# Optimization experiments

Measured on AMD Instinct MI355X. Metric: run time of the kernel, lower is better.

## Reference

```python
import jax, jax.numpy as jnp
import numpy as np

XY = 16   # xy_size
Z = 16    # z_size
S = XY * XY * Z   # num_states = 4096
V = 2048  # num_tokens


def _build_structure():
    # Static 3D-grid neighbor structure (replaces the per-state Python loop).
    h = np.arange(S)
    zc, rem = np.divmod(h, XY * XY)
    yc, xc = np.divmod(rem, XY)
    coords = np.stack([xc, yc, zc], 1)                       # [S,3] (x,y,z)
    offs = np.array([[0, 0, 0], [1, 0, 0], [-1, 0, 0], [0, 1, 0],
                     [0, -1, 0], [0, 0, 1], [0, 0, 2]])       # 7 fixed offsets
    nc = coords[:, None, :] + offs[None]                      # [S,7,3]
    valid = ((nc[..., 0] >= 0) & (nc[..., 0] < XY) &
             (nc[..., 1] >= 0) & (nc[..., 1] < XY) &
             (nc[..., 2] >= 0) & (nc[..., 2] < Z))
    dest = nc[..., 0] + XY * (nc[..., 1] + XY * nc[..., 2])   # flat neighbor idx
    # compact valid neighbors to the front, preserving offset order:
    # j-th valid neighbor consumes logit j (matches logits[h, :len(valid)])
    order = np.argsort(~valid, axis=1, kind='stable')
    tgt = np.take_along_axis(dest, order, axis=1)
    vmask = np.take_along_axis(valid, order, axis=1)
    tgt = np.where(vmask, tgt, S)  # invalid slots -> dummy column S
    return jnp.asarray(tgt), jnp.asarray(vmask)

TGT, VMASK = _build_structure()


def transition_log_p(trans_w):
    # masked log-softmax over the first k valid logits of each row
    logits = jnp.where(VMASK, trans_w, -1e30)
    logp = jax.nn.log_softmax(logits, axis=1)
    logp = jnp.where(VMASK, logp, -jnp.inf)
    T = jnp.full((S, S + 1), -jnp.inf, trans_w.dtype)
    T = T.at[jnp.arange(S)[:, None], TGT].set(logp)
    return T[:, :S]  # [S,S], row h = log p(transition targets of h)


def smoothed_emission(emis_w):
    em = jax.nn.log_softmax(emis_w, axis=-1).reshape(Z, XY, XY, V)
    lv, rv = em[:, :, :1], em[:, :, -1:]
    lh, rh = em[:, :1], em[:, -1:]
    c = jnp.zeros((Z, 1, 1, V), em.dtype)  # log(1)=0 pad, as in the original
    c2 = lambda *a: jnp.concatenate(a, axis=2)
    c1 = lambda *a: jnp.concatenate(a, axis=1)
    up = c1(c2(lv, em, rv), c2(c, rh, c), c2(c, rh, c))
    dn = c1(c2(c, lh, c), c2(c, lh, c), c2(lv, em, rv))
    lf = c1(c2(lh, c, c), c2(em, rv, rv), c2(rh, c, c))
    rt = c1(c2(c, c, lh), c2(lv, lv, em), c2(c, c, rh))
    cr = c1(c2(c, lh, c), c2(lv, em, rv), c2(c, rh, c))
    mean = jax.nn.logsumexp(jnp.stack((up, dn, lf, rt, cr)), axis=0) - jnp.log(5.0)
    return mean[:, 1:-1, 1:-1].reshape(S, V)


def _forward(stories, trans_w, emis_w, prior_w):
    priors = jax.nn.log_softmax(prior_w)                      # [S]
    em = smoothed_emission(emis_w)                            # [S,V]
    padded = jnp.concatenate([em, jnp.zeros((S, 1), em.dtype)], axis=1)  # [S,V+1]
    # per-(story, step) emission log-prob: sum over sentence tokens
    all_emis = padded.T[stories].sum(axis=2)                  # [B,L,S]
    all_emis = jnp.transpose(all_emis, (1, 0, 2))             # [L,B,S]
    T = transition_log_p(trans_w)                             # [S,S]
    amax = jnp.max(T, axis=1, keepdims=True)                  # [S,1], finite (self-loop)
    P = jnp.exp(T - amax)                                     # [S,S]
    score0 = all_emis[0] + priors                             # [B,S]

    def step(score, em_t):
        # new[b,a] = em_t[b,a] + logsumexp_h(T[a,h] + score[b,h])  (stable log-matmul)
        smax = jnp.max(score, axis=1, keepdims=True)          # [B,1]
        new = em_t + jnp.log(jnp.exp(score - smax) @ P.T) + smax + amax.T
        return new, new

    _, rest = jax.lax.scan(step, score0, all_emis[1:])
    return jnp.concatenate([score0[None], rest], axis=0)      # [L,B,S]


def setup_inputs() -> dict:
    key = jax.random.key(0)
    k1, k2, k3, k4 = jax.random.split(key, 4)
    B, L, W = 8, 32, 8
    return {
        "stories_tensor": jax.random.randint(k1, (B, L, W), 0, V + 1, dtype=jnp.int32),
        "story_length": L,
        "trans_w": jax.random.normal(k2, (S, 7), jnp.float32),
        "emis_w": jax.random.normal(k3, (S, V), jnp.float32),
        "prior_w": jax.random.normal(k4, (S,), jnp.float32),
    }


def reference(stories_tensor, story_length, trans_w, emis_w, prior_w):
    assert stories_tensor.shape[1] == story_length
    return _forward(stories_tensor, trans_w, emis_w, prior_w)
```

## Files before the change

### kernel.cpp

```cpp
#include <hip/hip_runtime.h>
#include <math.h>

#define XYD 16
#define ZD 16
#define SS 4096
#define VV 2048
#define BB 8
#define LL 32
#define WW 8
#define VC 32
#define SM_STRIDE 257

#define GUARD_L 16
#define GUARD_R 512
#define EBUF_N (GUARD_L + SS + GUARD_R)

#define BAR() asm volatile("s_waitcnt lgkmcnt(0)\n\ts_barrier" ::: "memory")

__device__ __forceinline__ float b2f(unsigned short u) {
    union { unsigned int i; float f; } x; x.i = ((unsigned int)u) << 16; return x.f;
}
__device__ __forceinline__ unsigned short f2b(float f) {
    union { float f; unsigned int i; } x; x.f = f; return (unsigned short)(x.i >> 16);
}

__global__ void k_logZ(const float* __restrict__ emis_w, float* __restrict__ logZ) {
    int wave = threadIdx.x >> 6;
    int lane = threadIdx.x & 63;
    int row  = blockIdx.x * 4 + wave;
    const float* r = emis_w + (size_t)row * VV;
    float vals[32];
    float m = -INFINITY;
#pragma unroll
    for (int k = 0; k < 8; k++) {
        float4 f = ((const float4*)r)[k * 64 + lane];
        vals[k*4+0] = f.x; vals[k*4+1] = f.y; vals[k*4+2] = f.z; vals[k*4+3] = f.w;
    }
#pragma unroll
    for (int k = 0; k < 32; k++) m = fmaxf(m, vals[k]);
#pragma unroll
    for (int o = 32; o; o >>= 1) m = fmaxf(m, __shfl_xor(m, o));
    float sum = 0.f;
#pragma unroll
    for (int k = 0; k < 32; k++) sum += __expf(vals[k] - m);
#pragma unroll
    for (int o = 32; o; o >>= 1) sum += __shfl_xor(sum, o);
    if (lane == 0) logZ[row] = m + __logf(sum);
}

__global__ void k_smooth(const float* __restrict__ emis_w, const float* __restrict__ logZ,
                         unsigned short* __restrict__ smTb) {
    __shared__ float tileT[VC * SM_STRIDE];
    int z  = blockIdx.x;
    int v0 = blockIdx.y * VC;
    int tid = threadIdx.x;
    int rsub = tid >> 3;
    int c0   = (tid & 7) * 4;

#pragma unroll
    for (int it = 0; it < 8; it++) {
        int r  = it * 32 + rsub;
        int sg = z * 256 + r;
        float lz = logZ[sg];
        float4 w = *(const float4*)(emis_w + (size_t)sg * VV + v0 + c0);
        tileT[(c0+0)*SM_STRIDE + r] = __expf(w.x - lz);
        tileT[(c0+1)*SM_STRIDE + r] = __expf(w.y - lz);
        tileT[(c0+2)*SM_STRIDE + r] = __expf(w.z - lz);
        tileT[(c0+3)*SM_STRIDE + r] = __expf(w.w - lz);
    }
    __syncthreads();

    int x = tid & 15, y = tid >> 4;
    int sxp = (x < 15) ? tid + 1  : tid;
    int sxm = (x > 0)  ? tid - 1  : tid;
    int syp = (y < 15) ? tid + 16 : tid;
    int sym = (y > 0)  ? tid - 16 : tid;
    unsigned short* o = smTb + (size_t)v0 * SS + z * 256 + tid;
#pragma unroll
    for (int i = 0; i < VC; i++) {
        const float* tb = tileT + i * SM_STRIDE;
        float s = tb[tid] + tb[sxp] + tb[sxm] + tb[syp] + tb[sym];
        o[(size_t)i * SS] = f2b(__logf(s * 0.2f));
    }
}

__global__ void __launch_bounds__(1024) k_forward(
    const float* __restrict__ trans_w, const float* __restrict__ prior_w,
    const unsigned short* __restrict__ smTb, const int* __restrict__ stories,
    float* __restrict__ out) {
    __shared__ __align__(16) unsigned short Ebuf[2][EBUF_N];
    __shared__ float red2[2];
    __shared__ float pr[16];
    __shared__ int toksL[LL * WW];
    int b = blockIdx.x;
    int tid = threadIdx.x;
    int lane = tid & 63, wid = tid >> 6;

    if (tid < GUARD_L) { Ebuf[0][tid] = 0; Ebuf[1][tid] = 0; }
    if (tid < GUARD_R) {
        Ebuf[0][GUARD_L + SS + tid] = 0;
        Ebuf[1][GUARD_L + SS + tid] = 0;
    }
    if (tid < LL * WW) toksL[tid] = stories[b * LL * WW + tid];

    float pw[28], am[4];
    {
        float w7[28];
        const float4* t4 = (const float4*)(trans_w + (size_t)tid * 28);
#pragma unroll
        for (int k = 0; k < 7; k++) ((float4*)w7)[k] = t4[k];
#pragma unroll
        for (int i = 0; i < 4; i++) {
            int j = tid * 4 + i;
            int xx = j & 15, yy = (j >> 4) & 15, zz = j >> 8;
            bool val[7];
            val[0] = true;
            val[1] = (xx < 15); val[2] = (xx > 0);
            val[3] = (yy < 15); val[4] = (yy > 0);
            val[5] = (zz < 15); val[6] = (zz < 14);
            const float* rw = w7 + i * 7;
            float w[7]; int cnt = 0; float m = -INFINITY;
#pragma unroll
            for (int d = 0; d < 7; d++) { if (val[d]) { w[d] = rw[cnt++]; m = fmaxf(m, w[d]); } }
            float se = 0.f;
#pragma unroll
            for (int d = 0; d < 7; d++) if (val[d]) se += __expf(w[d] - m);
#pragma unroll
            for (int d = 0; d < 7; d++) pw[i*7+d] = val[d] ? __expf(w[d] - m) : 0.f;
            am[i] = -__logf(se);
        }
    }

    float4 pv = ((const float4*)prior_w)[tid];
    __syncthreads();

    const unsigned short* smBase = smTb + 4 * tid;
    float4 em = {0.f, 0.f, 0.f, 0.f};
#pragma unroll
    for (int w = 0; w < WW; w++) {
        int tk = toksL[w];
        if (tk < VV) {
            ushort4 u = *(const ushort4*)(smBase + (size_t)tk * SS);
            em.x += b2f(u.x); em.y += b2f(u.y); em.z += b2f(u.z); em.w += b2f(u.w);
        }
    }

    float lm = fmaxf(fmaxf(pv.x, pv.y), fmaxf(pv.z, pv.w));
#pragma unroll
    for (int o = 32; o; o >>= 1) lm = fmaxf(lm, __shfl_xor(lm, o));
    if (lane == 0) pr[wid] = lm;
    __syncthreads();
    float gm = pr[0];
#pragma unroll
    for (int w = 1; w < 16; w++) gm = fmaxf(gm, pr[w]);
    __syncthreads();
    float ls = __expf(pv.x - gm) + __expf(pv.y - gm) + __expf(pv.z - gm) + __expf(pv.w - gm);
#pragma unroll
    for (int o = 32; o; o >>= 1) ls += __shfl_xor(ls, o);
    if (lane == 0) pr[wid] = ls;
    __syncthreads();
    float gs = 0.f;
#pragma unroll
    for (int w = 0; w < 16; w++) gs += pr[w];
    float logZp = gm + __logf(gs);

    float v0 = em.x + pv.x - logZp;
    float v1 = em.y + pv.y - logZp;
    float v2 = em.z + pv.z - logZp;
    float v3 = em.w + pv.w - logZp;
    float4 ov_prev = {v0, v1, v2, v3};
    float4* outp = (float4*)(out + (size_t)b * SS) + tid;

    if (tid == 0) red2[0] = v0;
    __syncthreads();
    float g1 = red2[0];
    float XpPrev = g1;
    float E0 = __expf(v0 - XpPrev), E1 = __expf(v1 - XpPrev);
    float E2 = __expf(v2 - XpPrev), E3 = __expf(v3 - XpPrev);
    {
        ushort4 E;
        E.x = f2b(E0); E.y = f2b(E1); E.z = f2b(E2); E.w = f2b(E3);
        *(ushort4*)(&Ebuf[0][GUARD_L + 4 * tid]) = E;
    }

    ushort4 pf[WW];
#pragma unroll
    for (int w = 0; w < WW; w++) {
        int tk = toksL[WW + w];
        pf[w] = (tk < VV) ? *(const ushort4*)(smBase + (size_t)tk * SS)
                          : (ushort4){0, 0, 0, 0};
    }

    int cur = 0;
    for (int t = 1; t < LL; t++) {
        BAR();
        em.x = 0.f; em.y = 0.f; em.z = 0.f; em.w = 0.f;
#pragma unroll
        for (int w = 0; w < WW; w++) {
            em.x += b2f(pf[w].x); em.y += b2f(pf[w].y);
            em.z += b2f(pf[w].z); em.w += b2f(pf[w].w);
        }
        if (t < LL - 1) {
#pragma unroll
            for (int w = 0; w < WW; w++) {
                int tk = toksL[(t + 1) * WW + w];
                pf[w] = (tk < VV) ? *(const ushort4*)(smBase + (size_t)tk * SS)
                                  : (ushort4){0, 0, 0, 0};
            }
        }

        float g0 = red2[cur];
        float Xp = 2.f * g0 - g1;
        float dX = XpPrev - Xp;
        float F0 = __expf(em.x + am[0] + dX);
        float F1 = __expf(em.y + am[1] + dX);
        float F2 = __expf(em.z + am[2] + dX);
        float F3 = __expf(em.w + am[3] + dX);

        *outp = ov_prev;
        outp += (BB * SS) / 4;

        const unsigned short* Eb = Ebuf[cur] + GUARD_L + 4 * tid;
        ushort4 YpU = *(const ushort4*)(Eb + 16);
        ushort4 YmU = *(const ushort4*)(Eb - 16);
        ushort4 ZpU = *(const ushort4*)(Eb + 256);
        ushort4 ZqU = *(const ushort4*)(Eb + 512);
        float bx  = b2f(Eb[4]);
        float cxw = b2f(Eb[-1]);

        float a0 = E0*pw[0]  + E1*pw[1]  + cxw*pw[2] + b2f(YpU.x)*pw[3]  + b2f(YmU.x)*pw[4]  + b2f(ZpU.x)*pw[5]  + b2f(ZqU.x)*pw[6];
        float a1 = E1*pw[7]  + E2*pw[8]  + E0*pw[9]  + b2f(YpU.y)*pw[10] + b2f(YmU.y)*pw[11] + b2f(ZpU.y)*pw[12] + b2f(ZqU.y)*pw[13];
        float a2 = E2*pw[14] + E3*pw[15] + E1*pw[16] + b2f(YpU.z)*pw[17] + b2f(YmU.z)*pw[18] + b2f(ZpU.z)*pw[19] + b2f(ZqU.z)*pw[20];
        float a3 = E3*pw[21] + bx*pw[22] + E2*pw[23] + b2f(YpU.w)*pw[24] + b2f(YmU.w)*pw[25] + b2f(ZpU.w)*pw[26] + b2f(ZqU.w)*pw[27];

        E0 = a0 * F0; E1 = a1 * F1; E2 = a2 * F2; E3 = a3 * F3;
        {
            ushort4 E;
            E.x = f2b(E0); E.y = f2b(E1); E.z = f2b(E2); E.w = f2b(E3);
            *(ushort4*)(&Ebuf[cur ^ 1][GUARD_L + 4 * tid]) = E;
        }
        float lg0 = __logf(a0);
        if (tid == 0) red2[cur ^ 1] = em.x + lg0 + XpPrev + am[0];

        ov_prev.x = em.x + lg0        + XpPrev + am[0];
        ov_prev.y = em.y + __logf(a1) + XpPrev + am[1];
        ov_prev.z = em.z + __logf(a2) + XpPrev + am[2];
        ov_prev.w = em.w + __logf(a3) + XpPrev + am[3];

        g1 = g0; XpPrev = Xp; cur ^= 1;
    }
    *outp = ov_prev;
}

extern "C" void kernel_launch(void* const* d_in, const int* in_sizes, int n_in,
                              void* d_out, int out_size, void* d_ws, size_t ws_size,
                              hipStream_t stream) {
    const int*   stories = (const int*)d_in[0];
    const float* trans_w = (const float*)d_in[2];
    const float* emis_w  = (const float*)d_in[3];
    const float* prior_w = (const float*)d_in[4];
    float* out = (float*)d_out;

    char* ws = (char*)d_ws;
    unsigned short* smTb = (unsigned short*)(ws);
    float* logZ = (float*)(ws + (size_t)VV * SS * 2);

    k_logZ<<<SS / 4, 256, 0, stream>>>(emis_w, logZ);
    k_smooth<<<dim3(ZD, VV / VC), 256, 0, stream>>>(emis_w, logZ, smTb);
    k_forward<<<BB, 1024, 0, stream>>>(trans_w, prior_w, smTb, stories, out);
}
```

Before: 183.7 us.

## Fuse all stages into one cooperative kernel with grid syncs and precomputed emissions

Replaces three kernel launches with a single cooperative kernel of 256 blocks that runs logZ, the smoothing transpose and an emission gather across the whole grid, separated by grid.sync. The per-timestep emission sums are computed in parallel by all blocks into a workspace buffer, so the sequential forward loop on 8 blocks only reads one float4 per step instead of gathering eight bf16 rows. This removes launch gaps and takes the gather off the serial critical path. In exchange it adds grid-wide barriers, a requirement that all 256 blocks of 1024 threads be co-resident, and an extra global write and read of all emissions.

After: 247.1 us. 34.5% more time.

```diff
diff --git a/kernel.cpp b/kernel.cpp
--- a/kernel.cpp
+++ b/kernel.cpp
@@ -1,5 +1,8 @@
 #include <hip/hip_runtime.h>
+#include <hip/hip_cooperative_groups.h>
 #include <math.h>
+
+namespace cg = cooperative_groups;
 
 #define XYD 16
 #define ZD 16
@@ -24,232 +27,237 @@
     union { float f; unsigned int i; } x; x.f = f; return (unsigned short)(x.i >> 16);
 }
 
-__global__ void k_logZ(const float* __restrict__ emis_w, float* __restrict__ logZ) {
-    int wave = threadIdx.x >> 6;
-    int lane = threadIdx.x & 63;
-    int row  = blockIdx.x * 4 + wave;
-    const float* r = emis_w + (size_t)row * VV;
-    float vals[32];
-    float m = -INFINITY;
-#pragma unroll
-    for (int k = 0; k < 8; k++) {
-        float4 f = ((const float4*)r)[k * 64 + lane];
-        vals[k*4+0] = f.x; vals[k*4+1] = f.y; vals[k*4+2] = f.z; vals[k*4+3] = f.w;
-    }
-#pragma unroll
-    for (int k = 0; k < 32; k++) m = fmaxf(m, vals[k]);
-#pragma unroll
-    for (int o = 32; o; o >>= 1) m = fmaxf(m, __shfl_xor(m, o));
-    float sum = 0.f;
-#pragma unroll
-    for (int k = 0; k < 32; k++) sum += __expf(vals[k] - m);
-#pragma unroll
-    for (int o = 32; o; o >>= 1) sum += __shfl_xor(sum, o);
-    if (lane == 0) logZ[row] = m + __logf(sum);
-}
-
-__global__ void k_smooth(const float* __restrict__ emis_w, const float* __restrict__ logZ,
-                         unsigned short* __restrict__ smTb) {
-    __shared__ float tileT[VC * SM_STRIDE];
-    int z  = blockIdx.x;
-    int v0 = blockIdx.y * VC;
-    int tid = threadIdx.x;
-    int rsub = tid >> 3;
-    int c0   = (tid & 7) * 4;
-
-#pragma unroll
-    for (int it = 0; it < 8; it++) {
-        int r  = it * 32 + rsub;
-        int sg = z * 256 + r;
-        float lz = logZ[sg];
-        float4 w = *(const float4*)(emis_w + (size_t)sg * VV + v0 + c0);
-        tileT[(c0+0)*SM_STRIDE + r] = __expf(w.x - lz);
-        tileT[(c0+1)*SM_STRIDE + r] = __expf(w.y - lz);
-        tileT[(c0+2)*SM_STRIDE + r] = __expf(w.z - lz);
-        tileT[(c0+3)*SM_STRIDE + r] = __expf(w.w - lz);
-    }
-    __syncthreads();
-
-    int x = tid & 15, y = tid >> 4;
-    int sxp = (x < 15) ? tid + 1  : tid;
-    int sxm = (x > 0)  ? tid - 1  : tid;
-    int syp = (y < 15) ? tid + 16 : tid;
-    int sym = (y > 0)  ? tid - 16 : tid;
-    unsigned short* o = smTb + (size_t)v0 * SS + z * 256 + tid;
-#pragma unroll
-    for (int i = 0; i < VC; i++) {
-        const float* tb = tileT + i * SM_STRIDE;
-        float s = tb[tid] + tb[sxp] + tb[sxm] + tb[syp] + tb[sym];
-        o[(size_t)i * SS] = f2b(__logf(s * 0.2f));
-    }
-}
-
-__global__ void __launch_bounds__(1024) k_forward(
-    const float* __restrict__ trans_w, const float* __restrict__ prior_w,
-    const unsigned short* __restrict__ smTb, const int* __restrict__ stories,
-    float* __restrict__ out) {
-    __shared__ __align__(16) unsigned short Ebuf[2][EBUF_N];
-    __shared__ float red2[2];
-    __shared__ float pr[16];
-    __shared__ int toksL[LL * WW];
-    int b = blockIdx.x;
-    int tid = threadIdx.x;
+__global__ void __launch_bounds__(1024, 4) k_all(
+    const int* __restrict__ stories, const float* __restrict__ trans_w,
+    const float* __restrict__ emis_w, const float* __restrict__ prior_w,
+    float* __restrict__ out, unsigned short* __restrict__ smTb,
+    float* __restrict__ all_emis, float* __restrict__ logZ) {
+
+    __shared__ __align__(16) char shraw[VC * SM_STRIDE * sizeof(float)];
+
+    cg::grid_group grid = cg::this_grid();
+    int tid = threadIdx.x, bid = blockIdx.x;
     int lane = tid & 63, wid = tid >> 6;
 
-    if (tid < GUARD_L) { Ebuf[0][tid] = 0; Ebuf[1][tid] = 0; }
-    if (tid < GUARD_R) {
-        Ebuf[0][GUARD_L + SS + tid] = 0;
-        Ebuf[1][GUARD_L + SS + tid] = 0;
-    }
-    if (tid < LL * WW) toksL[tid] = stories[b * LL * WW + tid];
-
-    float pw[28], am[4];
-    {
-        float w7[28];
-        const float4* t4 = (const float4*)(trans_w + (size_t)tid * 28);
-#pragma unroll
-        for (int k = 0; k < 7; k++) ((float4*)w7)[k] = t4[k];
-#pragma unroll
-        for (int i = 0; i < 4; i++) {
-            int j = tid * 4 + i;
-            int xx = j & 15, yy = (j >> 4) & 15, zz = j >> 8;
-            bool val[7];
-            val[0] = true;
-            val[1] = (xx < 15); val[2] = (xx > 0);
-            val[3] = (yy < 15); val[4] = (yy > 0);
-            val[5] = (zz < 15); val[6] = (zz < 14);
-            const float* rw = w7 + i * 7;
-            float w[7]; int cnt = 0; float m = -INFINITY;
-#pragma unroll
-            for (int d = 0; d < 7; d++) { if (val[d]) { w[d] = rw[cnt++]; m = fmaxf(m, w[d]); } }
-            float se = 0.f;
-#pragma unroll
-            for (int d = 0; d < 7; d++) if (val[d]) se += __expf(w[d] - m);
-#pragma unroll
-            for (int d = 0; d < 7; d++) pw[i*7+d] = val[d] ? __expf(w[d] - m) : 0.f;
-            am[i] = -__logf(se);
-        }
-    }
-
-    float4 pv = ((const float4*)prior_w)[tid];
-    __syncthreads();
-
-    const unsigned short* smBase = smTb + 4 * tid;
-    float4 em = {0.f, 0.f, 0.f, 0.f};
-#pragma unroll
-    for (int w = 0; w < WW; w++) {
-        int tk = toksL[w];
-        if (tk < VV) {
-            ushort4 u = *(const ushort4*)(smBase + (size_t)tk * SS);
-            em.x += b2f(u.x); em.y += b2f(u.y); em.z += b2f(u.z); em.w += b2f(u.w);
-        }
-    }
-
-    float lm = fmaxf(fmaxf(pv.x, pv.y), fmaxf(pv.z, pv.w));
-#pragma unroll
-    for (int o = 32; o; o >>= 1) lm = fmaxf(lm, __shfl_xor(lm, o));
-    if (lane == 0) pr[wid] = lm;
-    __syncthreads();
-    float gm = pr[0];
-#pragma unroll
-    for (int w = 1; w < 16; w++) gm = fmaxf(gm, pr[w]);
-    __syncthreads();
-    float ls = __expf(pv.x - gm) + __expf(pv.y - gm) + __expf(pv.z - gm) + __expf(pv.w - gm);
-#pragma unroll
-    for (int o = 32; o; o >>= 1) ls += __shfl_xor(ls, o);
-    if (lane == 0) pr[wid] = ls;
-    __syncthreads();
-    float gs = 0.f;
-#pragma unroll
-    for (int w = 0; w < 16; w++) gs += pr[w];
-    float logZp = gm + __logf(gs);
-
-    float v0 = em.x + pv.x - logZp;
-    float v1 = em.y + pv.y - logZp;
-    float v2 = em.z + pv.z - logZp;
-    float v3 = em.w + pv.w - logZp;
-    float4 ov_prev = {v0, v1, v2, v3};
-    float4* outp = (float4*)(out + (size_t)b * SS) + tid;
-
-    if (tid == 0) red2[0] = v0;
-    __syncthreads();
-    float g1 = red2[0];
-    float XpPrev = g1;
-    float E0 = __expf(v0 - XpPrev), E1 = __expf(v1 - XpPrev);
-    float E2 = __expf(v2 - XpPrev), E3 = __expf(v3 - XpPrev);
-    {
-        ushort4 E;
-        E.x = f2b(E0); E.y = f2b(E1); E.z = f2b(E2); E.w = f2b(E3);
-        *(ushort4*)(&Ebuf[0][GUARD_L + 4 * tid]) = E;
-    }
-
-    ushort4 pf[WW];
-#pragma unroll
-    for (int w = 0; w < WW; w++) {
-        int tk = toksL[WW + w];
-        pf[w] = (tk < VV) ? *(const ushort4*)(smBase + (size_t)tk * SS)
-                          : (ushort4){0, 0, 0, 0};
-    }
-
-    int cur = 0;
-    for (int t = 1; t < LL; t++) {
-        BAR();
-        em.x = 0.f; em.y = 0.f; em.z = 0.f; em.w = 0.f;
+    {
+        int row = bid * 16 + wid;
+        const float* r = emis_w + (size_t)row * VV;
+        float vals[32];
+        float m = -INFINITY;
+#pragma unroll
+        for (int k = 0; k < 8; k++) {
+            float4 f = ((const float4*)r)[k * 64 + lane];
+            vals[k*4+0] = f.x; vals[k*4+1] = f.y; vals[k*4+2] = f.z; vals[k*4+3] = f.w;
+        }
+#pragma unroll
+        for (int k = 0; k < 32; k++) m = fmaxf(m, vals[k]);
+#pragma unroll
+        for (int o = 32; o; o >>= 1) m = fmaxf(m, __shfl_xor(m, o));
+        float sum = 0.f;
+#pragma unroll
+        for (int k = 0; k < 32; k++) sum += __expf(vals[k] - m);
+#pragma unroll
+        for (int o = 32; o; o >>= 1) sum += __shfl_xor(sum, o);
+        if (lane == 0) logZ[row] = m + __logf(sum);
+    }
+    grid.sync();
+
+    {
+        float* tileT = (float*)shraw;
+        int rsub = tid >> 3;
+        int c0   = (tid & 7) * 4;
+        int s    = tid & 255, g = tid >> 8;
+        int x = s & 15, y = s >> 4;
+        int sxp = (x < 15) ? s + 1  : s;
+        int sxm = (x > 0)  ? s - 1  : s;
+        int syp = (y < 15) ? s + 16 : s;
+        int sym = (y > 0)  ? s - 16 : s;
+#pragma unroll
+        for (int c = 0; c < 4; c++) {
+            int combo = bid * 4 + c;
+            int z  = combo >> 6;
+            int v0 = (combo & 63) * VC;
+            __syncthreads();
+#pragma unroll
+            for (int it = 0; it < 2; it++) {
+                int r  = it * 128 + rsub;
+                int sg = z * 256 + r;
+                float lz = logZ[sg];
+                float4 w = *(const float4*)(emis_w + (size_t)sg * VV + v0 + c0);
+                tileT[(c0+0)*SM_STRIDE + r] = __expf(w.x - lz);
+                tileT[(c0+1)*SM_STRIDE + r] = __expf(w.y - lz);
+                tileT[(c0+2)*SM_STRIDE + r] = __expf(w.z - lz);
+                tileT[(c0+3)*SM_STRIDE + r] = __expf(w.w - lz);
+            }
+            __syncthreads();
+            unsigned short* o = smTb + (size_t)(v0 + g * 8) * SS + z * 256 + s;
+#pragma unroll
+            for (int i = 0; i < 8; i++) {
+                const float* tb = tileT + (g * 8 + i) * SM_STRIDE;
+                float sm = tb[s] + tb[sxp] + tb[sxm] + tb[syp] + tb[sym];
+                o[(size_t)i * SS] = f2b(__logf(sm * 0.2f));
+            }
+        }
+    }
+    grid.sync();
+
+    {
+        int t = bid >> 3, b = bid & 7;
+        int tok[WW];
+#pragma unroll
+        for (int w = 0; w < WW; w++) tok[w] = stories[(b * LL + t) * WW + w];
+        int s0 = tid * 4;
+        float4 acc = {0.f, 0.f, 0.f, 0.f};
 #pragma unroll
         for (int w = 0; w < WW; w++) {
-            em.x += b2f(pf[w].x); em.y += b2f(pf[w].y);
-            em.z += b2f(pf[w].z); em.w += b2f(pf[w].w);
-        }
-        if (t < LL - 1) {
-#pragma unroll
-            for (int w = 0; w < WW; w++) {
-                int tk = toksL[(t + 1) * WW + w];
-                pf[w] = (tk < VV) ? *(const ushort4*)(smBase + (size_t)tk * SS)
-                                  : (ushort4){0, 0, 0, 0};
-            }
-        }
-
-        float g0 = red2[cur];
-        float Xp = 2.f * g0 - g1;
-        float dX = XpPrev - Xp;
-        float F0 = __expf(em.x + am[0] + dX);
-        float F1 = __expf(em.y + am[1] + dX);
-        float F2 = __expf(em.z + am[2] + dX);
-        float F3 = __expf(em.w + am[3] + dX);
-
-        *outp = ov_prev;
-        outp += (BB * SS) / 4;
-
-        const unsigned short* Eb = Ebuf[cur] + GUARD_L + 4 * tid;
-        ushort4 YpU = *(const ushort4*)(Eb + 16);
-        ushort4 YmU = *(const ushort4*)(Eb - 16);
-        ushort4 ZpU = *(const ushort4*)(Eb + 256);
-        ushort4 ZqU = *(const ushort4*)(Eb + 512);
-        float bx  = b2f(Eb[4]);
-        float cxw = b2f(Eb[-1]);
-
-        float a0 = E0*pw[0]  + E1*pw[1]  + cxw*pw[2] + b2f(YpU.x)*pw[3]  + b2f(YmU.x)*pw[4]  + b2f(ZpU.x)*pw[5]  + b2f(ZqU.x)*pw[6];
-        float a1 = E1*pw[7]  + E2*pw[8]  + E0*pw[9]  + b2f(YpU.y)*pw[10] + b2f(YmU.y)*pw[11] + b2f(ZpU.y)*pw[12] + b2f(ZqU.y)*pw[13];
-        float a2 = E2*pw[14] + E3*pw[15] + E1*pw[16] + b2f(YpU.z)*pw[17] + b2f(YmU.z)*pw[18] + b2f(ZpU.z)*pw[19] + b2f(ZqU.z)*pw[20];
-        float a3 = E3*pw[21] + bx*pw[22] + E2*pw[23] + b2f(YpU.w)*pw[24] + b2f(YmU.w)*pw[25] + b2f(ZpU.w)*pw[26] + b2f(ZqU.w)*pw[27];
-
-        E0 = a0 * F0; E1 = a1 * F1; E2 = a2 * F2; E3 = a3 * F3;
+            if (tok[w] < VV) {
+                ushort4 u = *(const ushort4*)(smTb + (size_t)tok[w] * SS + s0);
+                acc.x += b2f(u.x); acc.y += b2f(u.y);
+                acc.z += b2f(u.z); acc.w += b2f(u.w);
+            }
+        }
+        *(float4*)(all_emis + ((size_t)t * BB + b) * SS + s0) = acc;
+    }
+    grid.sync();
+
+    if (bid >= BB) return;
+    {
+        unsigned short* Eb0 = (unsigned short*)shraw;
+        unsigned short* Eb1 = Eb0 + EBUF_N;
+        float* red2 = (float*)(shraw + 4 * EBUF_N);
+        float* pr   = red2 + 2;
+        int b = bid;
+
+        if (tid < GUARD_L) { Eb0[tid] = 0; Eb1[tid] = 0; }
+        if (tid < GUARD_R) {
+            Eb0[GUARD_L + SS + tid] = 0;
+            Eb1[GUARD_L + SS + tid] = 0;
+        }
+
+        float pw[28], am[4];
+        {
+            float w7[28];
+            const float4* t4 = (const float4*)(trans_w + (size_t)tid * 28);
+#pragma unroll
+            for (int k = 0; k < 7; k++) ((float4*)w7)[k] = t4[k];
+#pragma unroll
+            for (int i = 0; i < 4; i++) {
+                int j = tid * 4 + i;
+                int xx = j & 15, yy = (j >> 4) & 15, zz = j >> 8;
+                bool val[7];
+                val[0] = true;
+                val[1] = (xx < 15); val[2] = (xx > 0);
+                val[3] = (yy < 15); val[4] = (yy > 0);
+                val[5] = (zz < 15); val[6] = (zz < 14);
+                const float* rw = w7 + i * 7;
+                float w[7]; int cnt = 0; float m = -INFINITY;
+#pragma unroll
+                for (int d = 0; d < 7; d++) { if (val[d]) { w[d] = rw[cnt++]; m = fmaxf(m, w[d]); } }
+                float se = 0.f;
+#pragma unroll
+                for (int d = 0; d < 7; d++) if (val[d]) se += __expf(w[d] - m);
+#pragma unroll
+                for (int d = 0; d < 7; d++) pw[i*7+d] = val[d] ? __expf(w[d] - m) : 0.f;
+                am[i] = -__logf(se);
+            }
+        }
+
+        float4 pv = ((const float4*)prior_w)[tid];
+        const float4* emp = (const float4*)(all_emis + (size_t)b * SS) + tid;
+        float4 em = *emp;
+
+        float lm = fmaxf(fmaxf(pv.x, pv.y), fmaxf(pv.z, pv.w));
+#pragma unroll
+        for (int o = 32; o; o >>= 1) lm = fmaxf(lm, __shfl_xor(lm, o));
+        if (lane == 0) pr[wid] = lm;
+        __syncthreads();
+        float gm = pr[0];
+#pragma unroll
+        for (int w = 1; w < 16; w++) gm = fmaxf(gm, pr[w]);
+        __syncthreads();
+        float ls = __expf(pv.x - gm) + __expf(pv.y - gm) + __expf(pv.z - gm) + __expf(pv.w - gm);
+#pragma unroll
+        for (int o = 32; o; o >>= 1) ls += __shfl_xor(ls, o);
+        if (lane == 0) pr[wid] = ls;
+        __syncthreads();
+        float gs = 0.f;
+#pragma unroll
+        for (int w = 0; w < 16; w++) gs += pr[w];
+        float logZp = gm + __logf(gs);
+
+        float v0 = em.x + pv.x - logZp;
+        float v1 = em.y + pv.y - logZp;
+        float v2 = em.z + pv.z - logZp;
+        float v3 = em.w + pv.w - logZp;
+        float4 ov_prev = {v0, v1, v2, v3};
+        float4* outp = (float4*)(out + (size_t)b * SS) + tid;
+
+        if (tid == 0) red2[0] = v0;
+        __syncthreads();
+        float g1 = red2[0];
+        float XpPrev = g1;
+        float E0 = __expf(v0 - XpPrev), E1 = __expf(v1 - XpPrev);
+        float E2 = __expf(v2 - XpPrev), E3 = __expf(v3 - XpPrev);
         {
             ushort4 E;
             E.x = f2b(E0); E.y = f2b(E1); E.z = f2b(E2); E.w = f2b(E3);
-            *(ushort4*)(&Ebuf[cur ^ 1][GUARD_L + 4 * tid]) = E;
-        }
-        float lg0 = __logf(a0);
-        if (tid == 0) red2[cur ^ 1] = em.x + lg0 + XpPrev + am[0];
-
-        ov_prev.x = em.x + lg0        + XpPrev + am[0];
-        ov_prev.y = em.y + __logf(a1) + XpPrev + am[1];
-        ov_prev.z = em.z + __logf(a2) + XpPrev + am[2];
-        ov_prev.w = em.w + __logf(a3) + XpPrev + am[3];
-
-        g1 = g0; XpPrev = Xp; cur ^= 1;
-    }
-    *outp = ov_prev;
+            *(ushort4*)(&Eb0[GUARD_L + 4 * tid]) = E;
+        }
+
+        emp += (BB * SS) / 4;
+        float4 em_next = *emp;
+
+        unsigned short* Ec = Eb0;
+        unsigned short* En = Eb1;
+        int cur = 0;
+        for (int t = 1; t < LL; t++) {
+            BAR();
+            em = em_next;
+            if (t < LL - 1) { emp += (BB * SS) / 4; em_next = *emp; }
+
+            float g0 = red2[cur];
+            float Xp = 2.f * g0 - g1;
+            float dX = XpPrev - Xp;
+            float F0 = __expf(em.x + am[0] + dX);
+            float F1 = __expf(em.y + am[1] + dX);
+            float F2 = __expf(em.z + am[2] + dX);
+            float F3 = __expf(em.w + am[3] + dX);
+
+            *outp = ov_prev;
+            outp += (BB * SS) / 4;
+
+            const unsigned short* Eg = Ec + GUARD_L + 4 * tid;
+            ushort4 YpU = *(const ushort4*)(Eg + 16);
+            ushort4 YmU = *(const ushort4*)(Eg - 16);
+            ushort4 ZpU = *(const ushort4*)(Eg + 256);
+            ushort4 ZqU = *(const ushort4*)(Eg + 512);
+            float bx  = b2f(Eg[4]);
+            float cxw = b2f(Eg[-1]);
+
+            float a0 = E0*pw[0]  + E1*pw[1]  + cxw*pw[2] + b2f(YpU.x)*pw[3]  + b2f(YmU.x)*pw[4]  + b2f(ZpU.x)*pw[5]  + b2f(ZqU.x)*pw[6];
+            float a1 = E1*pw[7]  + E2*pw[8]  + E0*pw[9]  + b2f(YpU.y)*pw[10] + b2f(YmU.y)*pw[11] + b2f(ZpU.y)*pw[12] + b2f(ZqU.y)*pw[13];
+            float a2 = E2*pw[14] + E3*pw[15] + E1*pw[16] + b2f(YpU.z)*pw[17] + b2f(YmU.z)*pw[18] + b2f(ZpU.z)*pw[19] + b2f(ZqU.z)*pw[20];
+            float a3 = E3*pw[21] + bx*pw[22] + E2*pw[23] + b2f(YpU.w)*pw[24] + b2f(YmU.w)*pw[25] + b2f(ZpU.w)*pw[26] + b2f(ZqU.w)*pw[27];
+
+            E0 = a0 * F0; E1 = a1 * F1; E2 = a2 * F2; E3 = a3 * F3;
+            {
+                ushort4 E;
+                E.x = f2b(E0); E.y = f2b(E1); E.z = f2b(E2); E.w = f2b(E3);
+                *(ushort4*)(&En[GUARD_L + 4 * tid]) = E;
+            }
+            float lg0 = __logf(a0);
+            if (tid == 0) red2[cur ^ 1] = em.x + lg0 + XpPrev + am[0];
+
+            ov_prev.x = em.x + lg0        + XpPrev + am[0];
+            ov_prev.y = em.y + __logf(a1) + XpPrev + am[1];
+            ov_prev.z = em.z + __logf(a2) + XpPrev + am[2];
+            ov_prev.w = em.w + __logf(a3) + XpPrev + am[3];
+
+            g1 = g0; XpPrev = Xp; cur ^= 1;
+            unsigned short* tmp = Ec; Ec = En; En = tmp;
+        }
+        *outp = ov_prev;
+    }
 }
 
 extern "C" void kernel_launch(void* const* d_in, const int* in_sizes, int n_in,
@@ -263,9 +271,10 @@
 
     char* ws = (char*)d_ws;
     unsigned short* smTb = (unsigned short*)(ws);
-    float* logZ = (float*)(ws + (size_t)VV * SS * 2);
-
-    k_logZ<<<SS / 4, 256, 0, stream>>>(emis_w, logZ);
-    k_smooth<<<dim3(ZD, VV / VC), 256, 0, stream>>>(emis_w, logZ, smTb);
-    k_forward<<<BB, 1024, 0, stream>>>(trans_w, prior_w, smTb, stories, out);
-}
+    float* all_emis = (float*)(ws + (size_t)VV * SS * 2);
+    float* logZ     = (float*)(ws + (size_t)VV * SS * 2 + (size_t)LL * BB * SS * 4);
+
+    void* args[] = { (void*)&stories, (void*)&trans_w, (void*)&emis_w, (void*)&prior_w,
+                     (void*)&out, (void*)&smTb, (void*)&all_emis, (void*)&logZ };
+    hipLaunchCooperativeKernel((const void*)k_all, dim3(256), dim3(1024), args, 0, stream);
+}
```
